# Optimization experiments

Hardware: AMD Instinct MI355X
Metric: run time of the kernel (lower is better)

The kernel has to match this reference:

```python
import jax, jax.numpy as jnp
import numpy as np

D_MODEL = 768
N_HEADS = 12
HEAD_DIM = D_MODEL // N_HEADS
D_FF = 3072
LN_EPS = 1e-12


def layer_norm(x, gamma, beta, eps=LN_EPS):
    mu = jnp.mean(x, axis=-1, keepdims=True)
    var = jnp.var(x, axis=-1, keepdims=True)
    return (x - mu) * jax.lax.rsqrt(var + eps) * gamma + beta


def setup_inputs() -> dict:
    key = jax.random.key(0)
    ks = jax.random.split(key, 16)
    B, S = 4, 2048
    p = lambda k, shape: (jax.random.normal(k, shape, dtype=jnp.float32) * 0.02)
    return {
        "hidden_states": jax.random.normal(ks[0], (B, S, D_MODEL), dtype=jnp.float32),
        "Wq": p(ks[1], (D_MODEL, D_MODEL)), "bq": jnp.zeros((D_MODEL,), jnp.float32),
        "Wk": p(ks[2], (D_MODEL, D_MODEL)), "bk": jnp.zeros((D_MODEL,), jnp.float32),
        "Wv": p(ks[3], (D_MODEL, D_MODEL)), "bv": jnp.zeros((D_MODEL,), jnp.float32),
        "Wo": p(ks[4], (D_MODEL, D_MODEL)), "bo": jnp.zeros((D_MODEL,), jnp.float32),
        "ln1_g": jnp.ones((D_MODEL,), jnp.float32), "ln1_b": jnp.zeros((D_MODEL,), jnp.float32),
        "Wi": p(ks[5], (D_FF, D_MODEL)), "bi": jnp.zeros((D_FF,), jnp.float32),
        "Wf": p(ks[6], (D_MODEL, D_FF)), "bf": jnp.zeros((D_MODEL,), jnp.float32),
        "ln2_g": jnp.ones((D_MODEL,), jnp.float32), "ln2_b": jnp.zeros((D_MODEL,), jnp.float32),
    }


def reference(hidden_states, Wq, bq, Wk, bk, Wv, bv, Wo, bo, ln1_g, ln1_b,
              Wi, bi, Wf, bf, ln2_g, ln2_b):
    B, S, _ = hidden_states.shape
    # Q/K/V projections (computed as in source; outputs then overwritten by constants)
    q = hidden_states @ Wq.T + bq
    k = hidden_states @ Wk.T + bk
    v = hidden_states @ Wv.T + bv
    split = lambda x: x.reshape(B, S, N_HEADS, HEAD_DIM).transpose(0, 2, 1, 3)
    q, k, v = split(q), split(k), split(v)
    # source: torch.full_like(..., 0.01) overwrite of q/k/v
    q = jnp.full_like(q, 0.01)
    k = jnp.full_like(k, 0.01)
    v = jnp.full_like(v, 0.01)
    # naive attention: full [B,H,S,S] score matrix materialized
    scores = jnp.einsum("bhqd,bhkd->bhqk", q, k) / jnp.sqrt(jnp.float32(HEAD_DIM))
    probs = jax.nn.softmax(scores, axis=-1)
    ctx = jnp.einsum("bhqk,bhkd->bhqd", probs, v)
    ctx = ctx.transpose(0, 2, 1, 3).reshape(B, S, D_MODEL)
    # self-output: dense + residual + LayerNorm (dropout is identity in eval)
    attn_out = layer_norm(ctx @ Wo.T + bo + hidden_states, ln1_g, ln1_b)
    # FFN: fc1 + exact GELU, fc2 + residual + LayerNorm
    h = jax.nn.gelu(attn_out @ Wi.T + bi, approximate=False)
    layer_out = layer_norm(h @ Wf.T + bf + attn_out, ln2_g, ln2_b)
    return layer_out
```

## Files before the change

### kernel.cpp

```cpp
#include <hip/hip_runtime.h>
#include <hip/hip_bf16.h>
#include <cstdint>
#include <cstddef>


typedef __bf16 bf16;
typedef __attribute__((ext_vector_type(8))) __bf16 bf16x8;
typedef __attribute__((ext_vector_type(4))) __bf16 bf16x4;
typedef __attribute__((ext_vector_type(16))) float floatx16;

#define DM    768
#define DF    3072
#define MROWS 8192

#define N8          (DF * DM / 8)
#define CONV_BLOCKS (2 * N8 / 256)
#define CVEC_BLOCKS (DM / 4)

__device__ __forceinline__ void gl2lds16(const void* gp, void* lp) {
  __builtin_amdgcn_global_load_lds(
      (__attribute__((address_space(1))) void*)(void*)gp,
      (__attribute__((address_space(3))) void*)lp,
      16, 0, 0);
}

__device__ __forceinline__ float gelu_fast(float x) {
  float x2 = x * x;
  float m  = x * __builtin_fmaf(-0.1029641f, x2, -2.3025851f);
  float e  = __builtin_amdgcn_exp2f(m);
  return x * __builtin_amdgcn_rcpf(1.0f + e);
}

__global__ __launch_bounds__(256)
void prep_kernel(const float* __restrict__ Wi, const float* __restrict__ Wf,
                 bf16* __restrict__ Wib, bf16* __restrict__ Wfb,
                 const float* __restrict__ Wo, const float* __restrict__ bo,
                 float* __restrict__ cvec) {
  if (blockIdx.x < CONV_BLOCKS) {
    int i = blockIdx.x * 256 + threadIdx.x;
    const float* src = (i < N8) ? Wi : Wf;
    bf16* dst        = (i < N8) ? Wib : Wfb;
    int k            = (i < N8) ? i : i - N8;
    const float4* p = (const float4*)(src + (size_t)k * 8);
    float4 x = p[0], y = p[1];
    bf16x8 o;
    o[0]=(bf16)x.x; o[1]=(bf16)x.y; o[2]=(bf16)x.z; o[3]=(bf16)x.w;
    o[4]=(bf16)y.x; o[5]=(bf16)y.y; o[6]=(bf16)y.z; o[7]=(bf16)y.w;
    *(bf16x8*)(dst + (size_t)k * 8) = o;
  } else {
    int row  = (blockIdx.x - CONV_BLOCKS) * 4 + (threadIdx.x >> 6);
    int lane = threadIdx.x & 63;
    const float4* r = (const float4*)(Wo + (size_t)row * DM);
    float s = 0.f;
    #pragma unroll
    for (int t = 0; t < 3; ++t) {
      float4 v = r[lane + t * 64];
      s += v.x + v.y + v.z + v.w;
    }
    #pragma unroll
    for (int o = 32; o > 0; o >>= 1) s += __shfl_xor(s, o);
    if (lane == 0) cvec[row] = 0.01f * s + bo[row];
  }
}

__global__ __launch_bounds__(256)
void ln1_kernel(const float* __restrict__ hid, const float* __restrict__ cvec,
                const float* __restrict__ g, const float* __restrict__ b,
                bf16* __restrict__ out) {
  int row  = blockIdx.x * 4 + (threadIdx.x >> 6);
  int lane = threadIdx.x & 63;
  const float4* hrow = (const float4*)(hid + (size_t)row * DM);
  const float4* cv4  = (const float4*)cvec;
  float x[12];
  float s = 0.f, sq = 0.f;
  #pragma unroll
  for (int t = 0; t < 3; ++t) {
    int c = lane + t * 64;
    float4 v = hrow[c];
    float4 cc = cv4[c];
    float x0 = v.x + cc.x, x1 = v.y + cc.y, x2 = v.z + cc.z, x3 = v.w + cc.w;
    x[t*4+0] = x0; x[t*4+1] = x1; x[t*4+2] = x2; x[t*4+3] = x3;
    s  += x0 + x1 + x2 + x3;
    sq += x0*x0 + x1*x1 + x2*x2 + x3*x3;
  }
  #pragma unroll
  for (int o = 32; o > 0; o >>= 1) { s += __shfl_xor(s, o); sq += __shfl_xor(sq, o); }
  float mu  = s * (1.0f / DM);
  float var = sq * (1.0f / DM) - mu * mu;
  float inv = rsqrtf(var + 1e-12f);
  const float4* g4 = (const float4*)g;
  const float4* b4 = (const float4*)b;
  #pragma unroll
  for (int t = 0; t < 3; ++t) {
    int c = lane + t * 64;
    float4 gg = g4[c], bb = b4[c];
    bf16x4 o4;
    o4[0] = (bf16)((x[t*4+0] - mu) * inv * gg.x + bb.x);
    o4[1] = (bf16)((x[t*4+1] - mu) * inv * gg.y + bb.y);
    o4[2] = (bf16)((x[t*4+2] - mu) * inv * gg.z + bb.z);
    o4[3] = (bf16)((x[t*4+3] - mu) * inv * gg.w + bb.w);
    *(bf16x4*)(out + (size_t)row * DM + c * 4) = o4;
  }
}

__global__ __launch_bounds__(256)
void ln2_kernel(const bf16* __restrict__ p0, const bf16* __restrict__ p1,
                const float* __restrict__ bias, const bf16* __restrict__ attn,
                const float* __restrict__ g, const float* __restrict__ b,
                float* __restrict__ out) {
  int row  = blockIdx.x * 4 + (threadIdx.x >> 6);
  int lane = threadIdx.x & 63;
  const bf16* r0 = p0 + (size_t)row * DM;
  const bf16* r1 = p1 + (size_t)row * DM;
  const bf16* ar = attn + (size_t)row * DM;
  const float4* bi4 = (const float4*)bias;
  float x[12];
  float s = 0.f, sq = 0.f;
  #pragma unroll
  for (int t = 0; t < 3; ++t) {
    int c = lane + t * 64;
    bf16x4 a = *(const bf16x4*)(r0 + c * 4);
    bf16x4 d = *(const bf16x4*)(r1 + c * 4);
    bf16x4 rv = *(const bf16x4*)(ar + c * 4);
    float4 bb = bi4[c];
    float x0 = (float)a[0] + (float)d[0] + bb.x + (float)rv[0];
    float x1 = (float)a[1] + (float)d[1] + bb.y + (float)rv[1];
    float x2 = (float)a[2] + (float)d[2] + bb.z + (float)rv[2];
    float x3 = (float)a[3] + (float)d[3] + bb.w + (float)rv[3];
    x[t*4+0] = x0; x[t*4+1] = x1; x[t*4+2] = x2; x[t*4+3] = x3;
    s  += x0 + x1 + x2 + x3;
    sq += x0*x0 + x1*x1 + x2*x2 + x3*x3;
  }
  #pragma unroll
  for (int o = 32; o > 0; o >>= 1) { s += __shfl_xor(s, o); sq += __shfl_xor(sq, o); }
  float mu  = s * (1.0f / DM);
  float var = sq * (1.0f / DM) - mu * mu;
  float inv = rsqrtf(var + 1e-12f);
  const float4* g4 = (const float4*)g;
  const float4* b4 = (const float4*)b;
  float4* orow = (float4*)(out + (size_t)row * DM);
  #pragma unroll
  for (int t = 0; t < 3; ++t) {
    int c = lane + t * 64;
    float4 gg = g4[c], bb = b4[c];
    float4 o;
    o.x = (x[t*4+0] - mu) * inv * gg.x + bb.x;
    o.y = (x[t*4+1] - mu) * inv * gg.y + bb.y;
    o.z = (x[t*4+2] - mu) * inv * gg.z + bb.z;
    o.w = (x[t*4+3] - mu) * inv * gg.w + bb.w;
    orow[c] = o;
  }
}

#define BM 128
#define BN 128
#define BK 64
#define ES 136

template <int EPI>
__global__ __launch_bounds__(256, 4)
void gemm_nt(const bf16* __restrict__ A, const bf16* __restrict__ B,
             const float* __restrict__ bias,
             bf16* __restrict__ out, int M, int N, int K, int ksplit, int NB) {
  __shared__ __align__(16) unsigned char smem[BM * ES * 2];
  bf16* lds_a = (bf16*)smem;
  bf16* lds_b = lds_a + BM * BK;

  const int tid   = threadIdx.x;
  const int wave  = tid >> 6;
  const int lane  = tid & 63;
  const int l31   = lane & 31;
  const int lhi   = lane >> 5;
  const int xorv  = lane & 7;

  const int ygrp = blockIdx.x;
  const int xz   = blockIdx.y;
  const int xb   = xz % NB;
  const int zb   = xz / NB;

  const int m0 = ygrp * BM;
  const int n0 = xb * BN;
  const int wm = (wave >> 1) * 64;
  const int wn = (wave & 1) * 64;

  const int kbeg = zb * ksplit;
  const int kend = kbeg + ksplit;

  floatx16 acc[2][2] = {};
  const bf16* Ablk = A + (size_t)m0 * K;
  const bf16* Bblk = B + (size_t)n0 * K;

  for (int kk = kbeg; kk < kend; kk += BK) {
    #pragma unroll
    for (int i = 0; i < 4; ++i) {
      int ci  = tid + 256 * i;
      int r   = ci >> 3;
      int c_g = (ci & 7) ^ (r & 7);
      gl2lds16(Ablk + (size_t)r * K + kk + c_g * 8, lds_a + ci * 8);
      gl2lds16(Bblk + (size_t)r * K + kk + c_g * 8, lds_b + ci * 8);
    }
    __syncthreads();

    #pragma unroll
    for (int ks = 0; ks < BK; ks += 16) {
      const int cs = ((ks >> 3) + lhi) ^ xorv;
      bf16x8 af[2], bfr[2];
      #pragma unroll
      for (int i = 0; i < 2; ++i)
        af[i] = *(const bf16x8*)&lds_a[(wm + i * 32 + l31) * BK + cs * 8];
      #pragma unroll
      for (int j = 0; j < 2; ++j)
        bfr[j] = *(const bf16x8*)&lds_b[(wn + j * 32 + l31) * BK + cs * 8];
      #pragma unroll
      for (int i = 0; i < 2; ++i)
        #pragma unroll
        for (int j = 0; j < 2; ++j)
          acc[i][j] = __builtin_amdgcn_mfma_f32_32x32x16_bf16(af[i], bfr[j], acc[i][j], 0, 0, 0);
    }
    __syncthreads();
  }

  bf16* eb = (bf16*)smem;

  float bia[2];
  if constexpr (EPI == 0) {
    #pragma unroll
    for (int j = 0; j < 2; ++j) bia[j] = bias[n0 + wn + j * 32 + l31];
  }

  #pragma unroll
  for (int i = 0; i < 2; ++i) {
    #pragma unroll
    for (int j = 0; j < 2; ++j) {
      int col = wn + j * 32 + l31;
      #pragma unroll
      for (int r = 0; r < 16; ++r) {
        int row = wm + i * 32 + (r & 3) + 8 * (r >> 2) + 4 * lhi;
        float x = acc[i][j][r];
        if constexpr (EPI == 0) x = gelu_fast(x + bia[j]);
        eb[row * ES + col] = (bf16)x;
      }
    }
  }
  __syncthreads();

  bf16* outp = out + (EPI == 1 ? (size_t)zb * M * N : 0);
  const int rsub = tid >> 4;
  const int csub = (tid & 15) * 8;
  #pragma unroll
  for (int c = 0; c < 8; ++c) {
    int row = c * 16 + rsub;
    bf16x8 v = *(const bf16x8*)&eb[row * ES + csub];
    *(bf16x8*)&outp[(size_t)(m0 + row) * N + n0 + csub] = v;
  }
}

extern "C" void kernel_launch(void* const* d_in, const int* in_sizes, int n_in,
                              void* d_out, int out_size, void* d_ws, size_t ws_size,
                              hipStream_t stream) {
  (void)in_sizes; (void)n_in; (void)out_size; (void)ws_size;

  const float* hidden = (const float*)d_in[0];
  const float* Wo     = (const float*)d_in[7];
  const float* bo     = (const float*)d_in[8];
  const float* ln1_g  = (const float*)d_in[9];
  const float* ln1_b  = (const float*)d_in[10];
  const float* Wi     = (const float*)d_in[11];
  const float* bi     = (const float*)d_in[12];
  const float* Wf     = (const float*)d_in[13];
  const float* bf_    = (const float*)d_in[14];
  const float* ln2_g  = (const float*)d_in[15];
  const float* ln2_b  = (const float*)d_in[16];
  float* out = (float*)d_out;

  char* w = (char*)d_ws;
  float* cvec = (float*)w;
  size_t off = 4096;
  bf16* attn = (bf16*)(w + off); off += (size_t)MROWS * DM * 2;
  bf16* h    = (bf16*)(w + off); off += (size_t)MROWS * DF * 2;
  bf16* pre  = (bf16*)(w + off); off += (size_t)2 * MROWS * DM * 2;
  bf16* Wib  = (bf16*)(w + off); off += (size_t)DF * DM * 2;
  bf16* Wfb  = (bf16*)(w + off);

  prep_kernel<<<dim3(CONV_BLOCKS + CVEC_BLOCKS), dim3(256), 0, stream>>>(
      Wi, Wf, Wib, Wfb, Wo, bo, cvec);

  ln1_kernel<<<dim3(MROWS / 4), dim3(256), 0, stream>>>(hidden, cvec, ln1_g, ln1_b, attn);

  gemm_nt<0><<<dim3(MROWS / BM, DF / BN), dim3(256), 0, stream>>>(
      attn, Wib, bi, h, MROWS, DF, DM, DM, DF / BN);

  gemm_nt<1><<<dim3(MROWS / BM, (DM / BN) * 2), dim3(256), 0, stream>>>(
      h, Wfb, nullptr, pre, MROWS, DM, DF, DF / 2, DM / BN);

  ln2_kernel<<<dim3(MROWS / 4), dim3(256), 0, stream>>>(
      pre, pre + (size_t)MROWS * DM, bf_, attn, ln2_g, ln2_b, out);
}
```

Measured before the change: 226.1 us.

## Fuse first LayerNorm into the FC1 GEMM prologue, removing the ln1 launch

Removes the separate ln1 kernel. Each FC1 GEMM block now computes LayerNorm for its 128 rows, writes the bf16 result to the attn buffer, synchronises, and then runs its GEMM from that buffer. The goal is to save a kernel launch and the separate normalisation pass. In exchange, every one of the 24 column blocks sharing a row tile recomputes and rewrites the same LayerNorm rows. That adds a lot of redundant fp32 reads, bf16 writes and benign racing writes of identical data, plus a serial prologue before the MFMA loop.

```diff
diff --git a/kernel.cpp b/kernel.cpp
--- a/kernel.cpp
+++ b/kernel.cpp
@@ -64,46 +64,6 @@
 }
 
 __global__ __launch_bounds__(256)
-void ln1_kernel(const float* __restrict__ hid, const float* __restrict__ cvec,
-                const float* __restrict__ g, const float* __restrict__ b,
-                bf16* __restrict__ out) {
-  int row  = blockIdx.x * 4 + (threadIdx.x >> 6);
-  int lane = threadIdx.x & 63;
-  const float4* hrow = (const float4*)(hid + (size_t)row * DM);
-  const float4* cv4  = (const float4*)cvec;
-  float x[12];
-  float s = 0.f, sq = 0.f;
-  #pragma unroll
-  for (int t = 0; t < 3; ++t) {
-    int c = lane + t * 64;
-    float4 v = hrow[c];
-    float4 cc = cv4[c];
-    float x0 = v.x + cc.x, x1 = v.y + cc.y, x2 = v.z + cc.z, x3 = v.w + cc.w;
-    x[t*4+0] = x0; x[t*4+1] = x1; x[t*4+2] = x2; x[t*4+3] = x3;
-    s  += x0 + x1 + x2 + x3;
-    sq += x0*x0 + x1*x1 + x2*x2 + x3*x3;
-  }
-  #pragma unroll
-  for (int o = 32; o > 0; o >>= 1) { s += __shfl_xor(s, o); sq += __shfl_xor(sq, o); }
-  float mu  = s * (1.0f / DM);
-  float var = sq * (1.0f / DM) - mu * mu;
-  float inv = rsqrtf(var + 1e-12f);
-  const float4* g4 = (const float4*)g;
-  const float4* b4 = (const float4*)b;
-  #pragma unroll
-  for (int t = 0; t < 3; ++t) {
-    int c = lane + t * 64;
-    float4 gg = g4[c], bb = b4[c];
-    bf16x4 o4;
-    o4[0] = (bf16)((x[t*4+0] - mu) * inv * gg.x + bb.x);
-    o4[1] = (bf16)((x[t*4+1] - mu) * inv * gg.y + bb.y);
-    o4[2] = (bf16)((x[t*4+2] - mu) * inv * gg.z + bb.z);
-    o4[3] = (bf16)((x[t*4+3] - mu) * inv * gg.w + bb.w);
-    *(bf16x4*)(out + (size_t)row * DM + c * 4) = o4;
-  }
-}
-
-__global__ __launch_bounds__(256)
 void ln2_kernel(const bf16* __restrict__ p0, const bf16* __restrict__ p1,
                 const float* __restrict__ bias, const bf16* __restrict__ attn,
                 const float* __restrict__ g, const float* __restrict__ b,
@@ -157,11 +117,12 @@
 #define BK 64
 #define ES 136
 
-template <int EPI>
 __global__ __launch_bounds__(256, 4)
-void gemm_nt(const bf16* __restrict__ A, const bf16* __restrict__ B,
-             const float* __restrict__ bias,
-             bf16* __restrict__ out, int M, int N, int K, int ksplit, int NB) {
+void gemm1_ln(const float* __restrict__ hid, const float* __restrict__ cvec,
+              const float* __restrict__ g, const float* __restrict__ b,
+              bf16* __restrict__ attn,
+              const bf16* __restrict__ B, const float* __restrict__ bias,
+              bf16* __restrict__ out) {
   __shared__ __align__(16) unsigned char smem[BM * ES * 2];
   bf16* lds_a = (bf16*)smem;
   bf16* lds_b = lds_a + BM * BK;
@@ -174,23 +135,58 @@
   const int xorv  = lane & 7;
 
   const int ygrp = blockIdx.x;
-  const int xz   = blockIdx.y;
-  const int xb   = xz % NB;
-  const int zb   = xz / NB;
-
+  const int xb   = blockIdx.y;
   const int m0 = ygrp * BM;
   const int n0 = xb * BN;
   const int wm = (wave >> 1) * 64;
   const int wn = (wave & 1) * 64;
 
-  const int kbeg = zb * ksplit;
-  const int kend = kbeg + ksplit;
+  const int M = MROWS, N = DF, K = DM;
+
+  {
+    const float4* cv4 = (const float4*)cvec;
+    const float4* g4  = (const float4*)g;
+    const float4* b4  = (const float4*)b;
+    for (int rr = wave; rr < BM; rr += 4) {
+      int row = m0 + rr;
+      const float4* hrow = (const float4*)(hid + (size_t)row * DM);
+      float x[12];
+      float s = 0.f, sq = 0.f;
+      #pragma unroll
+      for (int t = 0; t < 3; ++t) {
+        int c = lane + t * 64;
+        float4 v = hrow[c];
+        float4 cc = cv4[c];
+        float x0 = v.x + cc.x, x1 = v.y + cc.y, x2 = v.z + cc.z, x3 = v.w + cc.w;
+        x[t*4+0] = x0; x[t*4+1] = x1; x[t*4+2] = x2; x[t*4+3] = x3;
+        s  += x0 + x1 + x2 + x3;
+        sq += x0*x0 + x1*x1 + x2*x2 + x3*x3;
+      }
+      #pragma unroll
+      for (int o = 32; o > 0; o >>= 1) { s += __shfl_xor(s, o); sq += __shfl_xor(sq, o); }
+      float mu  = s * (1.0f / DM);
+      float var = sq * (1.0f / DM) - mu * mu;
+      float inv = rsqrtf(var + 1e-12f);
+      #pragma unroll
+      for (int t = 0; t < 3; ++t) {
+        int c = lane + t * 64;
+        float4 gg = g4[c], bb = b4[c];
+        bf16x4 o4;
+        o4[0] = (bf16)((x[t*4+0] - mu) * inv * gg.x + bb.x);
+        o4[1] = (bf16)((x[t*4+1] - mu) * inv * gg.y + bb.y);
+        o4[2] = (bf16)((x[t*4+2] - mu) * inv * gg.z + bb.z);
+        o4[3] = (bf16)((x[t*4+3] - mu) * inv * gg.w + bb.w);
+        *(bf16x4*)(attn + (size_t)row * DM + c * 4) = o4;
+      }
+    }
+  }
+  __syncthreads();
 
   floatx16 acc[2][2] = {};
-  const bf16* Ablk = A + (size_t)m0 * K;
+  const bf16* Ablk = attn + (size_t)m0 * K;
   const bf16* Bblk = B + (size_t)n0 * K;
 
-  for (int kk = kbeg; kk < kend; kk += BK) {
+  for (int kk = 0; kk < K; kk += BK) {
     #pragma unroll
     for (int i = 0; i < 4; ++i) {
       int ci  = tid + 256 * i;
@@ -221,12 +217,9 @@
   }
 
   bf16* eb = (bf16*)smem;
-
   float bia[2];
-  if constexpr (EPI == 0) {
-    #pragma unroll
-    for (int j = 0; j < 2; ++j) bia[j] = bias[n0 + wn + j * 32 + l31];
-  }
+  #pragma unroll
+  for (int j = 0; j < 2; ++j) bia[j] = bias[n0 + wn + j * 32 + l31];
 
   #pragma unroll
   for (int i = 0; i < 2; ++i) {
@@ -236,15 +229,99 @@
       #pragma unroll
       for (int r = 0; r < 16; ++r) {
         int row = wm + i * 32 + (r & 3) + 8 * (r >> 2) + 4 * lhi;
-        float x = acc[i][j][r];
-        if constexpr (EPI == 0) x = gelu_fast(x + bia[j]);
-        eb[row * ES + col] = (bf16)x;
+        eb[row * ES + col] = (bf16)gelu_fast(acc[i][j][r] + bia[j]);
       }
     }
   }
   __syncthreads();
 
-  bf16* outp = out + (EPI == 1 ? (size_t)zb * M * N : 0);
+  const int rsub = tid >> 4;
+  const int csub = (tid & 15) * 8;
+  #pragma unroll
+  for (int c = 0; c < 8; ++c) {
+    int row = c * 16 + rsub;
+    bf16x8 v = *(const bf16x8*)&eb[row * ES + csub];
+    *(bf16x8*)&out[(size_t)(m0 + row) * N + n0 + csub] = v;
+  }
+}
+
+__global__ __launch_bounds__(256, 4)
+void gemm2_nt(const bf16* __restrict__ A, const bf16* __restrict__ B,
+              bf16* __restrict__ out, int M, int N, int K, int ksplit, int NB) {
+  __shared__ __align__(16) unsigned char smem[BM * ES * 2];
+  bf16* lds_a = (bf16*)smem;
+  bf16* lds_b = lds_a + BM * BK;
+
+  const int tid   = threadIdx.x;
+  const int wave  = tid >> 6;
+  const int lane  = tid & 63;
+  const int l31   = lane & 31;
+  const int lhi   = lane >> 5;
+  const int xorv  = lane & 7;
+
+  const int ygrp = blockIdx.x;
+  const int xz   = blockIdx.y;
+  const int xb   = xz % NB;
+  const int zb   = xz / NB;
+
+  const int m0 = ygrp * BM;
+  const int n0 = xb * BN;
+  const int wm = (wave >> 1) * 64;
+  const int wn = (wave & 1) * 64;
+
+  const int kbeg = zb * ksplit;
+  const int kend = kbeg + ksplit;
+
+  floatx16 acc[2][2] = {};
+  const bf16* Ablk = A + (size_t)m0 * K;
+  const bf16* Bblk = B + (size_t)n0 * K;
+
+  for (int kk = kbeg; kk < kend; kk += BK) {
+    #pragma unroll
+    for (int i = 0; i < 4; ++i) {
+      int ci  = tid + 256 * i;
+      int r   = ci >> 3;
+      int c_g = (ci & 7) ^ (r & 7);
+      gl2lds16(Ablk + (size_t)r * K + kk + c_g * 8, lds_a + ci * 8);
+      gl2lds16(Bblk + (size_t)r * K + kk + c_g * 8, lds_b + ci * 8);
+    }
+    __syncthreads();
+
+    #pragma unroll
+    for (int ks = 0; ks < BK; ks += 16) {
+      const int cs = ((ks >> 3) + lhi) ^ xorv;
+      bf16x8 af[2], bfr[2];
+      #pragma unroll
+      for (int i = 0; i < 2; ++i)
+        af[i] = *(const bf16x8*)&lds_a[(wm + i * 32 + l31) * BK + cs * 8];
+      #pragma unroll
+      for (int j = 0; j < 2; ++j)
+        bfr[j] = *(const bf16x8*)&lds_b[(wn + j * 32 + l31) * BK + cs * 8];
+      #pragma unroll
+      for (int i = 0; i < 2; ++i)
+        #pragma unroll
+        for (int j = 0; j < 2; ++j)
+          acc[i][j] = __builtin_amdgcn_mfma_f32_32x32x16_bf16(af[i], bfr[j], acc[i][j], 0, 0, 0);
+    }
+    __syncthreads();
+  }
+
+  bf16* eb = (bf16*)smem;
+  #pragma unroll
+  for (int i = 0; i < 2; ++i) {
+    #pragma unroll
+    for (int j = 0; j < 2; ++j) {
+      int col = wn + j * 32 + l31;
+      #pragma unroll
+      for (int r = 0; r < 16; ++r) {
+        int row = wm + i * 32 + (r & 3) + 8 * (r >> 2) + 4 * lhi;
+        eb[row * ES + col] = (bf16)acc[i][j][r];
+      }
+    }
+  }
+  __syncthreads();
+
+  bf16* outp = out + (size_t)zb * M * N;
   const int rsub = tid >> 4;
   const int csub = (tid & 15) * 8;
   #pragma unroll
@@ -285,13 +362,11 @@
   prep_kernel<<<dim3(CONV_BLOCKS + CVEC_BLOCKS), dim3(256), 0, stream>>>(
       Wi, Wf, Wib, Wfb, Wo, bo, cvec);
 
-  ln1_kernel<<<dim3(MROWS / 4), dim3(256), 0, stream>>>(hidden, cvec, ln1_g, ln1_b, attn);
-
-  gemm_nt<0><<<dim3(MROWS / BM, DF / BN), dim3(256), 0, stream>>>(
-      attn, Wib, bi, h, MROWS, DF, DM, DM, DF / BN);
-
-  gemm_nt<1><<<dim3(MROWS / BM, (DM / BN) * 2), dim3(256), 0, stream>>>(
-      h, Wfb, nullptr, pre, MROWS, DM, DF, DF / 2, DM / BN);
+  gemm1_ln<<<dim3(MROWS / BM, DF / BN), dim3(256), 0, stream>>>(
+      hidden, cvec, ln1_g, ln1_b, attn, Wib, bi, h);
+
+  gemm2_nt<<<dim3(MROWS / BM, (DM / BN) * 2), dim3(256), 0, stream>>>(
+      h, Wfb, pre, MROWS, DM, DF, DF / 2, DM / BN);
 
   ln2_kernel<<<dim3(MROWS / 4), dim3(256), 0, stream>>>(
       pre, pre + (size_t)MROWS * DM, bf_, attn, ln2_g, ln2_b, out);
```

Measured after the change: 282.4 us. 24.9% more time.
